# Performance work log

Measured on AMD Instinct MI355X. Metric: run time of the kernel, lower is better.

## Reference

```python
import jax, jax.numpy as jnp
import numpy as np

Nc, Nd, Ns = 8000, 6000, 6000          # circRNA / drug / disease node counts
F, H, O = 64, 4, 64                    # feature dim (fcir=fdrug=fdis), GAT heads, cnn out_channels
Ec, Ed, Es = 256000, 192000, 192000    # directed edge counts per graph
NEG_SLOPE = 0.2


def _gcn(x, src, dst, ew, W, b, N):
    # PyG GCNConv w/ edge_weight: add self loops (w=1), symmetric norm, x@W.T, scatter-add
    loop = jnp.arange(N, dtype=src.dtype)
    s = jnp.concatenate([src, loop])
    d = jnp.concatenate([dst, loop])
    w = jnp.concatenate([ew, jnp.ones((N,), x.dtype)])
    deg = jax.ops.segment_sum(w, d, num_segments=N)
    dinv = jnp.where(deg > 0, jax.lax.rsqrt(deg), 0.0)
    norm = dinv[s] * w * dinv[d]                        # [E+N]
    h = x @ W.T                                         # [N,F]
    return jax.ops.segment_sum(h[s] * norm[:, None], d, num_segments=N) + b


def _gat(x, src, dst, ew, W, a_src, a_dst, We, a_edge, b, N):
    # PyG GATConv(heads=H, concat=False, edge_dim=1); self loops with fill_value='mean'
    E = src.shape[0]
    ea = ew[:, None]                                    # [E,1]
    cnt = jax.ops.segment_sum(jnp.ones((E,), x.dtype), dst, num_segments=N)
    esum = jax.ops.segment_sum(ea, dst, num_segments=N)
    loop_attr = esum / jnp.maximum(cnt, 1.0)[:, None]   # per-dst mean edge attr
    loop = jnp.arange(N, dtype=src.dtype)
    s = jnp.concatenate([src, loop])
    d = jnp.concatenate([dst, loop])
    ea = jnp.concatenate([ea, loop_attr], axis=0)       # [E+N,1]
    h = (x @ W.T).reshape(N, H, F)
    al_s = jnp.einsum('nhf,hf->nh', h, a_src)
    al_d = jnp.einsum('nhf,hf->nh', h, a_dst)
    e = (ea @ We.T).reshape(-1, H, F)
    al_e = jnp.einsum('ehf,hf->eh', e, a_edge)
    alpha = al_s[s] + al_d[d] + al_e                    # [E+N,H]
    alpha = jnp.where(alpha >= 0, alpha, NEG_SLOPE * alpha)   # leaky_relu
    amax = jax.ops.segment_max(alpha, d, num_segments=N)
    ex = jnp.exp(alpha - amax[d])
    denom = jax.ops.segment_sum(ex, d, num_segments=N)
    coef = ex / denom[d]                                # segment softmax over incoming edges
    out = jax.ops.segment_sum(h[s] * coef[:, :, None], d, num_segments=N)  # [N,H,F]
    return out.mean(axis=1) + b                         # concat=False -> head mean


def _readout(x1, x2, W, b):
    # Conv1d(in=2, out=O, kernel=(F,1)) on [1,2,F,N] == full contraction over (layer, feature)
    X = jnp.stack([x1, x2], axis=0)                     # [2,N,F]
    return jnp.einsum('cnf,ocf->no', X, W) + b          # [N,O]


def _forward(fl, cir_edges, drug_edges, dis_edges):
    def branch(x, ei, ew, g1W, g1b, gaW, gas, gad, gaeW, gae, gab, g2W, g2b, N):
        src, dst = ei[0], ei[1]
        f1 = jax.nn.relu(_gcn(x, src, dst, ew, g1W, g1b, N))
        att = jax.nn.relu(_gat(f1, src, dst, ew, gaW, gas, gad, gaeW, gae, gab, N))
        f2 = jax.nn.relu(_gcn(att, src, dst, ew, g2W, g2b, N))
        return f1, f2

    cf1, cf2 = branch(fl['x_cir'], cir_edges, fl['cir_ew'], fl['gcn_cir1_W'], fl['gcn_cir1_b'],
                      fl['gat_cir_W'], fl['gat_cir_asrc'], fl['gat_cir_adst'], fl['gat_cir_eW'],
                      fl['gat_cir_aedge'], fl['gat_cir_b'], fl['gcn_cir2_W'], fl['gcn_cir2_b'], Nc)
    # NOTE: the source forward reuses the *_dis GCN/GAT layers for the drug branch (faithful)
    df1, df2 = branch(fl['x_drug'], drug_edges, fl['drug_ew'], fl['gcn_dis1_W'], fl['gcn_dis1_b'],
                      fl['gat_dis_W'], fl['gat_dis_asrc'], fl['gat_dis_adst'], fl['gat_dis_eW'],
                      fl['gat_dis_aedge'], fl['gat_dis_b'], fl['gcn_dis2_W'], fl['gcn_dis2_b'], Nd)
    sf1, sf2 = branch(fl['x_dis'], dis_edges, fl['dis_ew'], fl['gcn_dis1_W'], fl['gcn_dis1_b'],
                      fl['gat_dis_W'], fl['gat_dis_asrc'], fl['gat_dis_adst'], fl['gat_dis_eW'],
                      fl['gat_dis_aedge'], fl['gat_dis_b'], fl['gcn_dis2_W'], fl['gcn_dis2_b'], Ns)
    cir_fea = _readout(cf1, cf2, fl['cnn_cir_W'], fl['cnn_cir_b'])
    drug_fea = _readout(df1, df2, fl['cnn_dis_W'], fl['cnn_dis_b'])   # source uses cnn_dis for drug too
    dis_fea = _readout(sf1, sf2, fl['cnn_dis_W'], fl['cnn_dis_b'])
    return (cir_fea @ dis_fea.T, cir_fea @ drug_fea.T, drug_fea @ dis_fea.T,
            cir_fea, drug_fea, dis_fea)


_PARAM_SHAPES = [
    ('gcn_cir1_W', (F, F)), ('gcn_cir1_b', (F,)),
    ('gcn_cir2_W', (F, F)), ('gcn_cir2_b', (F,)),
    ('gcn_dis1_W', (F, F)), ('gcn_dis1_b', (F,)),
    ('gcn_dis2_W', (F, F)), ('gcn_dis2_b', (F,)),
    ('gat_cir_W', (H * F, F)), ('gat_cir_asrc', (H, F)), ('gat_cir_adst', (H, F)),
    ('gat_cir_eW', (H * F, 1)), ('gat_cir_aedge', (H, F)), ('gat_cir_b', (F,)),
    ('gat_dis_W', (H * F, F)), ('gat_dis_asrc', (H, F)), ('gat_dis_adst', (H, F)),
    ('gat_dis_eW', (H * F, 1)), ('gat_dis_aedge', (H, F)), ('gat_dis_b', (F,)),
    ('cnn_cir_W', (O, 2, F)), ('cnn_cir_b', (O,)),
    ('cnn_dis_W', (O, 2, F)), ('cnn_dis_b', (O,)),
]


def setup_inputs() -> dict:
    key = jax.random.key(0)
    ks = iter(jax.random.split(key, 64))
    inp = {}
    inp['x_cir'] = jax.random.normal(next(ks), (Nc, F), jnp.float32)
    inp['x_drug'] = jax.random.normal(next(ks), (Nd, F), jnp.float32)
    inp['x_dis'] = jax.random.normal(next(ks), (Ns, F), jnp.float32)
    inp['cir_edges'] = jax.random.randint(next(ks), (2, Ec), 0, Nc, dtype=jnp.int32)
    inp['cir_ew'] = jax.random.uniform(next(ks), (Ec,), jnp.float32)
    inp['drug_edges'] = jax.random.randint(next(ks), (2, Ed), 0, Nd, dtype=jnp.int32)
    inp['drug_ew'] = jax.random.uniform(next(ks), (Ed,), jnp.float32)
    inp['dis_edges'] = jax.random.randint(next(ks), (2, Es), 0, Ns, dtype=jnp.int32)
    inp['dis_ew'] = jax.random.uniform(next(ks), (Es,), jnp.float32)
    for name, shape in _PARAM_SHAPES:
        inp[name] = jax.random.normal(next(ks), shape, jnp.float32) * 0.1
    return inp


def reference(x_cir, x_drug, x_dis, cir_edges, cir_ew, drug_edges, drug_ew, dis_edges, dis_ew,
              gcn_cir1_W, gcn_cir1_b, gcn_cir2_W, gcn_cir2_b,
              gcn_dis1_W, gcn_dis1_b, gcn_dis2_W, gcn_dis2_b,
              gat_cir_W, gat_cir_asrc, gat_cir_adst, gat_cir_eW, gat_cir_aedge, gat_cir_b,
              gat_dis_W, gat_dis_asrc, gat_dis_adst, gat_dis_eW, gat_dis_aedge, gat_dis_b,
              cnn_cir_W, cnn_cir_b, cnn_dis_W, cnn_dis_b):
    fl = {k: v for k, v in locals().items() if k not in ('cir_edges', 'drug_edges', 'dis_edges')}
    return _forward(fl, cir_edges, drug_edges, dis_edges)
```

## Files before the change

### kernel.cpp

```cpp
#include <hip/hip_runtime.h>

#define NEG_SLOPE 0.2f

typedef __attribute__((ext_vector_type(8))) short bfrag;
typedef __attribute__((ext_vector_type(4))) float f32x4;

static __device__ __forceinline__ ushort f2bf(float x){
  uint u = __float_as_uint(x);
  uint r = (u + 0x7fff + ((u>>16)&1)) >> 16;
  return (ushort)r;
}
static __device__ __forceinline__ float bf2f(ushort h){
  return __uint_as_float(((uint)h)<<16);
}
static __device__ __forceinline__ float rdlane(float v, int l){
  return __int_as_float(__builtin_amdgcn_readlane(__float_as_int(v), l));
}


struct G3 {
  const int* src[3]; const int* dst[3]; const float* ew[3];
  float* deg[3];
  int* cnt[3]; int* pos[3];
  float* dinv[3]; float* lat[3]; int* rowp[3];
  int4* ep[3];
  int N[3]; int E[3];
};

struct MM3 {
  const float* A[3]; const float* B[3]; float* C[3]; const float* bias[3];
  ushort* H[3]; ushort* L[3];
  const float* gas[3]; const float* gad[3];
  float* als[3]; float* ald[3];
  int M[3]; int lda, ldb, N2;
};

struct AGG3 {
  const float* h[3]; const float* dinv[3]; const int* rowp[3];
  const int4* ep[3]; const float* bias[3];
  float* out[3]; int N[3]; int ostride, ooff;
};

struct GAT3 {
  const float* hg[3]; const float* als[3]; const float* ald[3];
  const float* lat[3]; const float* ce[3]; const int* rowp[3];
  const int4* ep[3]; const float* bias[3];
  float* out[3]; int N[3];
};

struct SC3 {
  const ushort* AH[3]; const ushort* AL[3];
  const ushort* BH[3]; const ushort* BL[3];
  float* C[3]; int M[3]; int N2;
};


__global__ void k_scan_b(G3 g, const float* gaeW_c, const float* gae_c, float* ce_c,
                         const float* gaeW_d, const float* gae_d, float* ce_d){
  int b = blockIdx.x;
  int tid = threadIdx.x;
  if (b < 2 && tid < 64){
    const float* W = b ? gaeW_d : gaeW_c;
    const float* Aa = b ? gae_d : gae_c;
    float* ceo = b ? ce_d : ce_c;
    #pragma unroll
    for (int hh=0; hh<4; hh++){
      float v = W[hh*64+tid] * Aa[hh*64+tid];
      #pragma unroll
      for (int off=32; off>0; off>>=1) v += __shfl_down(v,off);
      if (tid==0) ceo[hh] = v;
    }
  }
  int N = g.N[b];
  const float* degsum = g.deg[b];
  const int* cnt = g.cnt[b];
  float* dinv = g.dinv[b];
  float* lat = g.lat[b];
  int* rowp = g.rowp[b];
  const int T = 1024, PER = 8;
  __shared__ int ssum[T];
  int base = tid*PER;
  int loc[PER]; int s = 0;
  #pragma unroll
  for (int u=0;u<PER;u++){
    int i = base+u;
    int c = (i<N)? cnt[i] : 0;
    loc[u] = s; s += c;
    if (i<N){
      float ds = degsum[i];
      dinv[i] = rsqrtf(1.0f + ds);
      lat[i] = ds / fmaxf((float)c, 1.0f);
    }
  }
  ssum[tid] = s; __syncthreads();
  for (int off=1; off<T; off<<=1){
    int t = (tid>=off)? ssum[tid-off] : 0;
    __syncthreads();
    ssum[tid] += t;
    __syncthreads();
  }
  int excl = ssum[tid] - s;
  #pragma unroll
  for (int u=0;u<PER;u++){ int i=base+u; if (i<N) rowp[i] = excl + loc[u]; }
  if (tid == T-1) rowp[N] = ssum[T-1];
}

__global__ void k_scatter_b(G3 g){
  int b = blockIdx.z;
  int e = blockIdx.x*blockDim.x + threadIdx.x;
  if (e < g.E[b]){
    int d = g.dst[b][e];
    int s = g.src[b][e];
    float w = g.ew[b][e];
    float dw = g.dinv[b][s] * w;
    int p = g.rowp[b][d] + atomicAdd(&g.pos[b][d], 1);
    g.ep[b][p] = make_int4(s, __float_as_int(w), __float_as_int(dw), 0);
  }
}


template<int K, bool BIAS, bool SPLIT, bool ALQ, bool STATS>
__global__ __launch_bounds__(256)
void k_mm_b(MM3 P, G3 g){
  if (STATS && blockIdx.x == gridDim.x-1){
    int b = blockIdx.z;
    int E = g.E[b];
    const int* __restrict__ dst = g.dst[b];
    const float* __restrict__ ew = g.ew[b];
    float* __restrict__ deg = g.deg[b];
    int* __restrict__ cnt = g.cnt[b];
    int stride = gridDim.y*256;
    for (int e = blockIdx.y*256 + threadIdx.x; e < E; e += stride){
      int d = dst[e];
      atomicAdd(&deg[d], ew[e]);
      atomicAdd(&cnt[d], 1);
    }
    return;
  }
  int br = blockIdx.z;
  int M = P.M[br];
  int bi = blockIdx.y*128;
  if (bi >= M) return;
  int N2 = P.N2;
  int bj = blockIdx.x*128;
  const float* __restrict__ A = P.A[br];
  const float* __restrict__ B = P.B[br];
  float* __restrict__ C = P.C[br];
  int lda = P.lda, ldb = P.ldb;

  __shared__ float As[128*36];
  __shared__ float Bs[32*132];
  int tid = threadIdx.x;
  int tx = tid & 15, ty = tid >> 4;
  float acc[8][8] = {};

  for (int kh = 0; kh < K; kh += 32){
    for (int t = tid; t < 1024; t += 256){
      int r = t >> 3, k4 = (t & 7) << 2;
      int gr = bi + r;
      float4 v = (gr < M) ? *(const float4*)(A + (size_t)gr*lda + kh + k4)
                          : make_float4(0.f,0.f,0.f,0.f);
      *(float4*)(As + r*36 + k4) = v;
    }
    for (int t = tid; t < 1024; t += 256){
      int r = t >> 3, k4 = (t & 7) << 2;
      int gr = bj + r;
      float4 v = (gr < N2) ? *(const float4*)(B + (size_t)gr*ldb + kh + k4)
                           : make_float4(0.f,0.f,0.f,0.f);
      Bs[(k4+0)*132 + r] = v.x;
      Bs[(k4+1)*132 + r] = v.y;
      Bs[(k4+2)*132 + r] = v.z;
      Bs[(k4+3)*132 + r] = v.w;
    }
    __syncthreads();
    #pragma unroll
    for (int k = 0; k < 32; k += 4){
      float4 a4[8];
      #pragma unroll
      for (int u=0; u<4; u++){
        a4[u]   = *(const float4*)(As + (ty*4+u)*36 + k);
        a4[u+4] = *(const float4*)(As + (64+ty*4+u)*36 + k);
      }
      #pragma unroll
      for (int i=0; i<4; i++){
        float4 bl = *(const float4*)(Bs + (k+i)*132 + tx*4);
        float4 bh = *(const float4*)(Bs + (k+i)*132 + 64 + tx*4);
        #pragma unroll
        for (int u=0; u<8; u++){
          float av = (i==0)?a4[u].x : (i==1)?a4[u].y : (i==2)?a4[u].z : a4[u].w;
          acc[u][0] += av*bl.x; acc[u][1] += av*bl.y;
          acc[u][2] += av*bl.z; acc[u][3] += av*bl.w;
          acc[u][4] += av*bh.x; acc[u][5] += av*bh.y;
          acc[u][6] += av*bh.z; acc[u][7] += av*bh.w;
        }
      }
    }
    __syncthreads();
  }

  #pragma unroll
  for (int u=0; u<8; u++){
    int gi = bi + ((u<4) ? (ty*4+u) : (64+ty*4+(u-4)));
    if (gi >= M) continue;
    #pragma unroll
    for (int half=0; half<2; half++){
      int gj = bj + ((half==0) ? tx*4 : 64+tx*4);
      int v0 = half*4;
      if (gj + 4 <= N2){
        float4 r4 = make_float4(acc[u][v0],acc[u][v0+1],acc[u][v0+2],acc[u][v0+3]);
        if (BIAS){
          const float* bb = P.bias[br];
          r4.x += bb[gj]; r4.y += bb[gj+1]; r4.z += bb[gj+2]; r4.w += bb[gj+3];
        }
        *(float4*)(C + (size_t)gi*N2 + gj) = r4;
        if (SPLIT){
          ushort hv[4], lv[4];
          float vv[4] = {r4.x, r4.y, r4.z, r4.w};
          #pragma unroll
          for (int v=0; v<4; v++){
            hv[v] = f2bf(vv[v]);
            lv[v] = f2bf(vv[v] - bf2f(hv[v]));
          }
          *(ushort4*)(P.H[br] + (size_t)gi*N2 + gj) = make_ushort4(hv[0],hv[1],hv[2],hv[3]);
          *(ushort4*)(P.L[br] + (size_t)gi*N2 + gj) = make_ushort4(lv[0],lv[1],lv[2],lv[3]);
        }
      } else {
        for (int v=0; v<4; v++) if (gj+v < N2){
          float r = acc[u][v0+v];
          if (BIAS) r += P.bias[br][gj+v];
          C[(size_t)gi*N2+gj+v] = r;
        }
      }
    }
  }

  if (ALQ){
    int h0 = bj >> 6;
    float ps[8][2], pd[8][2];
    #pragma unroll
    for (int u=0;u<8;u++){ ps[u][0]=0.f; ps[u][1]=0.f; pd[u][0]=0.f; pd[u][1]=0.f; }
    #pragma unroll
    for (int half=0; half<2; half++){
      #pragma unroll
      for (int v=0; v<4; v++){
        int cw = tx*4 + v;
        float gs = P.gas[br][(h0+half)*64 + cw];
        float gd = P.gad[br][(h0+half)*64 + cw];
        #pragma unroll
        for (int u=0;u<8;u++){
          ps[u][half] += acc[u][half*4+v]*gs;
          pd[u][half] += acc[u][half*4+v]*gd;
        }
      }
    }
    #pragma unroll
    for (int u=0;u<8;u++){
      #pragma unroll
      for (int hf=0; hf<2; hf++){
        float s = ps[u][hf], d = pd[u][hf];
        #pragma unroll
        for (int off=8; off>0; off>>=1){ s += __shfl_down(s,off); d += __shfl_down(d,off); }
        if (tx==0){
          int gi = bi + ((u<4) ? (ty*4+u) : (64+ty*4+(u-4)));
          if (gi < M){
            P.als[br][gi*4 + h0 + hf] = s;
            P.ald[br][gi*4 + h0 + hf] = d;
          }
        }
      }
    }
  }
}


__global__ void k_gcn_agg_b(AGG3 P){
  int b = blockIdx.z;
  int wid = (blockIdx.x*blockDim.x + threadIdx.x) >> 6;
  int f = threadIdx.x & 63;
  if (wid >= P.N[b]) return;
  const float* __restrict__ h = P.h[b];
  const int4* __restrict__ ep = P.ep[b];
  float dn = P.dinv[b][wid];
  float acc = dn*h[(size_t)wid*64 + f];
  int p0 = P.rowp[b][wid], p1 = P.rowp[b][wid+1];
  int p = p0;
  for (; p+4 <= p1; p+=4){
    int4 e0 = ep[p], e1 = ep[p+1], e2 = ep[p+2], e3 = ep[p+3];
    float v0 = h[(size_t)e0.x*64 + f];
    float v1 = h[(size_t)e1.x*64 + f];
    float v2 = h[(size_t)e2.x*64 + f];
    float v3 = h[(size_t)e3.x*64 + f];
    acc = fmaf(__int_as_float(e0.z), v0, acc);
    acc = fmaf(__int_as_float(e1.z), v1, acc);
    acc = fmaf(__int_as_float(e2.z), v2, acc);
    acc = fmaf(__int_as_float(e3.z), v3, acc);
  }
  for (; p < p1; p++){
    int4 pr = ep[p];
    acc = fmaf(__int_as_float(pr.z), h[(size_t)pr.x*64 + f], acc);
  }
  P.out[b][(size_t)wid*P.ostride + P.ooff + f] = fmaxf(fmaf(dn, acc, P.bias[b][f]), 0.f);
}


__global__ void k_gat_agg_b(GAT3 P){
  int b = blockIdx.z;
  int wid = (blockIdx.x*blockDim.x + threadIdx.x) >> 6;
  int lane = threadIdx.x & 63;
  if (wid >= P.N[b]) return;
  const float* __restrict__ hg = P.hg[b];
  const float* __restrict__ als = P.als[b];
  const int4* __restrict__ ep = P.ep[b];
  int h = lane & 3;
  int el = lane >> 2;
  int f = lane;

  float4 cv = *(const float4*)P.ce[b];
  float4 adv = *(const float4*)(P.ald[b] + (size_t)wid*4);
  float4 asv = *(const float4*)(als + (size_t)wid*4);
  float c_l  = (h==0)?cv.x :(h==1)?cv.y :(h==2)?cv.z :cv.w;
  float ad_l = (h==0)?adv.x:(h==1)?adv.y:(h==2)?adv.z:adv.w;
  float as_l = (h==0)?asv.x:(h==1)?asv.y:(h==2)?asv.z:asv.w;
  float la = P.lat[b][wid];

  float a_self = as_l + ad_l + la*c_l;
  a_self = (a_self >= 0.f) ? a_self : NEG_SLOPE*a_self;
  float m = a_self;

  float l = 1.f;
  const float* hn = hg + (size_t)wid*256;
  float acc0 = hn[f];
  float acc1 = hn[64+f];
  float acc2 = hn[128+f];
  float acc3 = hn[192+f];

  int p0 = P.rowp[b][wid], p1 = P.rowp[b][wid+1];
  for (int c0=p0; c0<p1; c0+=16){
    int idx = c0 + el;
    float ex = 0.f;
    int s_lane = 0;
    if (idx < p1){
      int4 pr = ep[idx];
      s_lane = pr.x;
      float w = __int_as_float(pr.y);
      float a = als[s_lane*4 + h] + ad_l + w*c_l;
      a = (a >= 0.f) ? a : NEG_SLOPE*a;
      ex = __expf(a - m);
    }
    float ls = ex;
    #pragma unroll
    for (int off=4; off<64; off<<=1) ls += __shfl_xor(ls, off);
    l += ls;
    int cnt = p1 - c0; if (cnt > 16) cnt = 16;
    #pragma unroll 2
    for (int e=0; e<cnt; e++){
      int s = __builtin_amdgcn_readlane(s_lane, e*4);
      const float* hs = hg + (size_t)s*256 + f;
      float x0 = rdlane(ex, e*4+0);
      float x1 = rdlane(ex, e*4+1);
      float x2 = rdlane(ex, e*4+2);
      float x3 = rdlane(ex, e*4+3);
      acc0 = fmaf(x0, hs[0],   acc0);
      acc1 = fmaf(x1, hs[64],  acc1);
      acc2 = fmaf(x2, hs[128], acc2);
      acc3 = fmaf(x3, hs[192], acc3);
    }
  }
  float o = acc0/rdlane(l,0) + acc1/rdlane(l,1) + acc2/rdlane(l,2) + acc3/rdlane(l,3);
  P.out[b][(size_t)wid*64 + f] = fmaxf(0.25f*o + P.bias[b][f], 0.f);
}


__global__ __launch_bounds__(256)
void k_score(SC3 P){
  int br = blockIdx.z;
  int M = P.M[br];
  int bi = blockIdx.y*128;
  if (bi >= M) return;
  int N = P.N2;
  int bj = blockIdx.x*128;
  const ushort* __restrict__ AH = P.AH[br];
  const ushort* __restrict__ ALo = P.AL[br];
  const ushort* __restrict__ BH = P.BH[br];
  const ushort* __restrict__ BLo = P.BL[br];
  float* __restrict__ C = P.C[br];

  int wv = threadIdx.x >> 6;
  int lane = threadIdx.x & 63;
  int la = lane & 15, lk = lane >> 4;
  int r0 = bi + (wv>>1)*64;
  int c0 = bj + (wv&1)*64;

  bfrag ah[4][2], al[4][2];
  #pragma unroll
  for (int mi=0; mi<4; mi++){
    int r = r0 + mi*16 + la; if (r > M-1) r = M-1;
    size_t base = (size_t)r*64 + lk*8;
    ah[mi][0] = *(const bfrag*)(AH + base);
    ah[mi][1] = *(const bfrag*)(AH + base + 32);
    al[mi][0] = *(const bfrag*)(ALo + base);
    al[mi][1] = *(const bfrag*)(ALo + base + 32);
  }

  f32x4 acc[4][4];
  #pragma unroll
  for (int mi=0; mi<4; mi++)
    #pragma unroll
    for (int ni=0; ni<4; ni++)
      acc[mi][ni] = (f32x4){0.f,0.f,0.f,0.f};

  #pragma unroll
  for (int ni=0; ni<4; ni++){
    int cc = c0 + ni*16 + la; if (cc > N-1) cc = N-1;
    size_t base = (size_t)cc*64 + lk*8;
    bfrag bh0 = *(const bfrag*)(BH + base);
    bfrag bh1 = *(const bfrag*)(BH + base + 32);
    bfrag bl0 = *(const bfrag*)(BLo + base);
    bfrag bl1 = *(const bfrag*)(BLo + base + 32);
    #pragma unroll
    for (int mi=0; mi<4; mi++){
      f32x4 a = acc[mi][ni];
      a = __builtin_amdgcn_mfma_f32_16x16x32_bf16(ah[mi][0], bh0, a, 0, 0, 0);
      a = __builtin_amdgcn_mfma_f32_16x16x32_bf16(ah[mi][1], bh1, a, 0, 0, 0);
      a = __builtin_amdgcn_mfma_f32_16x16x32_bf16(ah[mi][0], bl0, a, 0, 0, 0);
      a = __builtin_amdgcn_mfma_f32_16x16x32_bf16(ah[mi][1], bl1, a, 0, 0, 0);
      a = __builtin_amdgcn_mfma_f32_16x16x32_bf16(al[mi][0], bh0, a, 0, 0, 0);
      a = __builtin_amdgcn_mfma_f32_16x16x32_bf16(al[mi][1], bh1, a, 0, 0, 0);
      acc[mi][ni] = a;
    }
  }

  #pragma unroll
  for (int mi=0; mi<4; mi++){
    int rb = r0 + mi*16 + lk*4;
    #pragma unroll
    for (int ni=0; ni<4; ni++){
      int col = c0 + ni*16 + la;
      if (col >= N) continue;
      #pragma unroll
      for (int rg=0; rg<4; rg++){
        int r = rb + rg;
        if (r < M) C[(size_t)r*N + col] = acc[mi][ni][rg];
      }
    }
  }
}


extern "C" void kernel_launch(void* const* d_in, const int* in_sizes, int n_in,
                              void* d_out, int out_size, void* d_ws, size_t ws_size,
                              hipStream_t stream){
  const float* x_cir  = (const float*)d_in[0];
  const float* x_drug = (const float*)d_in[1];
  const float* x_dis  = (const float*)d_in[2];
  const int*   cir_edges  = (const int*)d_in[3];
  const float* cir_ew     = (const float*)d_in[4];
  const int*   drug_edges = (const int*)d_in[5];
  const float* drug_ew    = (const float*)d_in[6];
  const int*   dis_edges  = (const int*)d_in[7];
  const float* dis_ew     = (const float*)d_in[8];
  const float* gcn_cir1_W = (const float*)d_in[9];
  const float* gcn_cir1_b = (const float*)d_in[10];
  const float* gcn_cir2_W = (const float*)d_in[11];
  const float* gcn_cir2_b = (const float*)d_in[12];
  const float* gcn_dis1_W = (const float*)d_in[13];
  const float* gcn_dis1_b = (const float*)d_in[14];
  const float* gcn_dis2_W = (const float*)d_in[15];
  const float* gcn_dis2_b = (const float*)d_in[16];
  const float* gat_cir_W    = (const float*)d_in[17];
  const float* gat_cir_asrc = (const float*)d_in[18];
  const float* gat_cir_adst = (const float*)d_in[19];
  const float* gat_cir_eW   = (const float*)d_in[20];
  const float* gat_cir_aedge= (const float*)d_in[21];
  const float* gat_cir_b    = (const float*)d_in[22];
  const float* gat_dis_W    = (const float*)d_in[23];
  const float* gat_dis_asrc = (const float*)d_in[24];
  const float* gat_dis_adst = (const float*)d_in[25];
  const float* gat_dis_eW   = (const float*)d_in[26];
  const float* gat_dis_aedge= (const float*)d_in[27];
  const float* gat_dis_b    = (const float*)d_in[28];
  const float* cnn_cir_W = (const float*)d_in[29];
  const float* cnn_cir_b = (const float*)d_in[30];
  const float* cnn_dis_W = (const float*)d_in[31];
  const float* cnn_dis_b = (const float*)d_in[32];
  float* out = (float*)d_out;

  const int Nb[3] = {8000, 6000, 6000};
  const int Eb[3] = {256000, 192000, 192000};

  char* wp = (char*)d_ws;
  auto alloc = [&](size_t bytes)->void*{
    void* p = wp; wp += (bytes + 255) & ~(size_t)255; return p;
  };

  float* fea[3] = { out + 132000000ULL, out + 132512000ULL, out + 132896000ULL };

  float* ce_c = (float*)alloc(64);
  float* ce_d = (float*)alloc(64);

  G3 g;
  const int* edges[3] = {cir_edges, drug_edges, dis_edges};
  const float* ews[3] = {cir_ew, drug_ew, dis_ew};

  char* zero_base = wp;
  for (int b=0; b<3; b++){
    g.deg[b]  = (float*)alloc((size_t)Nb[b]*4);
    g.cnt[b]  = (int*)alloc((size_t)Nb[b]*4);
    g.pos[b]  = (int*)alloc((size_t)Nb[b]*4);
  }
  size_t zero_bytes = (size_t)(wp - zero_base);

  float *hbuf[3], *f12[3], *att[3], *als[3], *ald[3];
  ushort *feaH[3], *feaL[3];
  for (int b=0; b<3; b++){
    g.src[b] = edges[b];
    g.dst[b] = edges[b] + Eb[b];
    g.ew[b]  = ews[b];
    g.N[b] = Nb[b]; g.E[b] = Eb[b];
    g.dinv[b] = (float*)alloc((size_t)Nb[b]*4);
    g.lat[b]  = (float*)alloc((size_t)Nb[b]*4);
    g.rowp[b] = (int*)alloc((size_t)(Nb[b]+1)*4);
    g.ep[b]   = (int4*)alloc((size_t)Eb[b]*16);
    als[b]  = (float*)alloc((size_t)Nb[b]*4*4);
    ald[b]  = (float*)alloc((size_t)Nb[b]*4*4);
    hbuf[b] = (float*)alloc((size_t)Nb[b]*256*4);
    f12[b]  = (float*)alloc((size_t)Nb[b]*128*4);
    att[b]  = (float*)alloc((size_t)Nb[b]*64*4);
    feaH[b] = (ushort*)alloc((size_t)Nb[b]*64*2);
    feaL[b] = (ushort*)alloc((size_t)Nb[b]*64*2);
  }

  const float* xin[3]  = {x_cir, x_drug, x_dis};
  const float* g1W[3]  = {gcn_cir1_W, gcn_dis1_W, gcn_dis1_W};
  const float* g1b[3]  = {gcn_cir1_b, gcn_dis1_b, gcn_dis1_b};
  const float* g2W[3]  = {gcn_cir2_W, gcn_dis2_W, gcn_dis2_W};
  const float* g2b[3]  = {gcn_cir2_b, gcn_dis2_b, gcn_dis2_b};
  const float* gaW[3]  = {gat_cir_W, gat_dis_W, gat_dis_W};
  const float* gasP[3] = {gat_cir_asrc, gat_dis_asrc, gat_dis_asrc};
  const float* gadP[3] = {gat_cir_adst, gat_dis_adst, gat_dis_adst};
  const float* gab[3]  = {gat_cir_b, gat_dis_b, gat_dis_b};
  const float* cep[3]  = {ce_c, ce_d, ce_d};
  const float* cW[3]   = {cnn_cir_W, cnn_dis_W, cnn_dis_W};
  const float* cb[3]   = {cnn_cir_b, cnn_dis_b, cnn_dis_b};

  auto mkmm = [&](MM3& m, const float* const* Ap, const float* const* Bp,
                  float* const* Cp, const float* const* bp, int lda, int ldb, int N2){
    for (int b=0;b<3;b++){
      m.A[b]=Ap[b]; m.B[b]=Bp[b]; m.C[b]=Cp[b]; m.bias[b]= bp? bp[b] : nullptr;
      m.H[b]=nullptr; m.L[b]=nullptr;
      m.gas[b]=nullptr; m.gad[b]=nullptr; m.als[b]=nullptr; m.ald[b]=nullptr;
      m.M[b]=Nb[b];
    }
    m.lda=lda; m.ldb=ldb; m.N2=N2;
  };

  hipMemsetAsync(zero_base, 0, zero_bytes, stream);

  MM3 m1; mkmm(m1, xin, g1W, hbuf, nullptr, 64, 64, 64);
  k_mm_b<64,false,false,false,true><<<dim3(2,63,3),256,0,stream>>>(m1, g);

  k_scan_b<<<3,1024,0,stream>>>(g, gat_cir_eW, gat_cir_aedge, ce_c,
                                   gat_dis_eW, gat_dis_aedge, ce_d);
  k_scatter_b<<<dim3(1000,1,3),256,0,stream>>>(g);

  AGG3 a1;
  for (int b=0;b<3;b++){ a1.h[b]=hbuf[b]; a1.dinv[b]=g.dinv[b]; a1.rowp[b]=g.rowp[b];
    a1.ep[b]=g.ep[b]; a1.bias[b]=g1b[b]; a1.out[b]=f12[b]; a1.N[b]=Nb[b]; }
  a1.ostride=128; a1.ooff=0;
  k_gcn_agg_b<<<dim3(2000,1,3),256,0,stream>>>(a1);

  {
    const float* Ap[3] = {f12[0], f12[1], f12[2]};
    MM3 m2; mkmm(m2, Ap, gaW, hbuf, nullptr, 128, 64, 256);
    for (int b=0;b<3;b++){ m2.gas[b]=gasP[b]; m2.gad[b]=gadP[b]; m2.als[b]=als[b]; m2.ald[b]=ald[b]; }
    k_mm_b<64,false,false,true,false><<<dim3(2,63,3),256,0,stream>>>(m2, g);
  }

  GAT3 gt;
  for (int b=0;b<3;b++){ gt.hg[b]=hbuf[b]; gt.als[b]=als[b]; gt.ald[b]=ald[b]; gt.lat[b]=g.lat[b];
    gt.ce[b]=cep[b]; gt.rowp[b]=g.rowp[b]; gt.ep[b]=g.ep[b];
    gt.bias[b]=gab[b]; gt.out[b]=att[b]; gt.N[b]=Nb[b]; }
  k_gat_agg_b<<<dim3(2000,1,3),256,0,stream>>>(gt);

  {
    const float* Ap[3] = {att[0], att[1], att[2]};
    MM3 m3; mkmm(m3, Ap, g2W, hbuf, nullptr, 64, 64, 64);
    k_mm_b<64,false,false,false,false><<<dim3(1,63,3),256,0,stream>>>(m3, g);
  }

  AGG3 a2 = a1;
  for (int b=0;b<3;b++){ a2.bias[b]=g2b[b]; }
  a2.ooff=64;
  k_gcn_agg_b<<<dim3(2000,1,3),256,0,stream>>>(a2);

  {
    const float* Ap[3] = {f12[0], f12[1], f12[2]};
    MM3 m4; mkmm(m4, Ap, cW, fea, cb, 128, 128, 64);
    for (int b=0;b<3;b++){ m4.H[b]=feaH[b]; m4.L[b]=feaL[b]; }
    k_mm_b<128,true,true,false,false><<<dim3(1,63,3),256,0,stream>>>(m4, g);
  }

  SC3 sc;
  sc.AH[0]=feaH[0]; sc.AL[0]=feaL[0]; sc.BH[0]=feaH[2]; sc.BL[0]=feaL[2];
  sc.C[0]=out;               sc.M[0]=8000;
  sc.AH[1]=feaH[0]; sc.AL[1]=feaL[0]; sc.BH[1]=feaH[1]; sc.BL[1]=feaL[1];
  sc.C[1]=out + 48000000ULL; sc.M[1]=8000;
  sc.AH[2]=feaH[1]; sc.AL[2]=feaL[1]; sc.BH[2]=feaH[2]; sc.BL[2]=feaL[2];
  sc.C[2]=out + 96000000ULL; sc.M[2]=6000;
  sc.N2=6000;
  k_score<<<dim3(47,63,3),256,0,stream>>>(sc);
}
```

Baseline: 992.3 us.

## Store GAT features in bf16 and coalesce score writes via shared memory

The GAT projection matmul now writes its output as bf16, and the GAT aggregation reads bf16 and widens to float, halving the bytes of the per-edge neighbour gathers. The score kernel now stages each wave's accumulator tile in shared memory and writes it out as row-contiguous float4 stores to improve write coalescing of the large output. This reduces precision of GAT features, and the score kernel now uses a large shared buffer per block, which may lower occupancy.

```diff
diff --git a/kernel.cpp b/kernel.cpp
--- a/kernel.cpp
+++ b/kernel.cpp
@@ -42,7 +42,8 @@
 };
 
 struct GAT3 {
-  const float* hg[3]; const float* als[3]; const float* ald[3];
+  const ushort* hg[3];
+  const float* als[3]; const float* ald[3];
   const float* lat[3]; const float* ce[3]; const int* rowp[3];
   const int4* ep[3]; const float* bias[3];
   float* out[3]; int N[3];
@@ -119,7 +120,7 @@
 }
 
 
-template<int K, bool BIAS, bool SPLIT, bool ALQ, bool STATS>
+template<int K, bool BIAS, bool SPLIT, bool ALQ, bool STATS, bool CBF>
 __global__ __launch_bounds__(256)
 void k_mm_b(MM3 P, G3 g){
   if (STATS && blockIdx.x == gridDim.x-1){
@@ -212,23 +213,29 @@
           const float* bb = P.bias[br];
           r4.x += bb[gj]; r4.y += bb[gj+1]; r4.z += bb[gj+2]; r4.w += bb[gj+3];
         }
-        *(float4*)(C + (size_t)gi*N2 + gj) = r4;
-        if (SPLIT){
-          ushort hv[4], lv[4];
-          float vv[4] = {r4.x, r4.y, r4.z, r4.w};
-          #pragma unroll
-          for (int v=0; v<4; v++){
-            hv[v] = f2bf(vv[v]);
-            lv[v] = f2bf(vv[v] - bf2f(hv[v]));
+        if (CBF){
+          ushort4 uv = make_ushort4(f2bf(r4.x), f2bf(r4.y), f2bf(r4.z), f2bf(r4.w));
+          *(ushort4*)((ushort*)C + (size_t)gi*N2 + gj) = uv;
+        } else {
+          *(float4*)(C + (size_t)gi*N2 + gj) = r4;
+          if (SPLIT){
+            ushort hv[4], lv[4];
+            float vv[4] = {r4.x, r4.y, r4.z, r4.w};
+            #pragma unroll
+            for (int v=0; v<4; v++){
+              hv[v] = f2bf(vv[v]);
+              lv[v] = f2bf(vv[v] - bf2f(hv[v]));
+            }
+            *(ushort4*)(P.H[br] + (size_t)gi*N2 + gj) = make_ushort4(hv[0],hv[1],hv[2],hv[3]);
+            *(ushort4*)(P.L[br] + (size_t)gi*N2 + gj) = make_ushort4(lv[0],lv[1],lv[2],lv[3]);
           }
-          *(ushort4*)(P.H[br] + (size_t)gi*N2 + gj) = make_ushort4(hv[0],hv[1],hv[2],hv[3]);
-          *(ushort4*)(P.L[br] + (size_t)gi*N2 + gj) = make_ushort4(lv[0],lv[1],lv[2],lv[3]);
         }
       } else {
         for (int v=0; v<4; v++) if (gj+v < N2){
           float r = acc[u][v0+v];
           if (BIAS) r += P.bias[br][gj+v];
-          C[(size_t)gi*N2+gj+v] = r;
+          if (CBF) ((ushort*)C)[(size_t)gi*N2+gj+v] = f2bf(r);
+          else     C[(size_t)gi*N2+gj+v] = r;
         }
       }
     }
@@ -308,7 +315,7 @@
   int wid = (blockIdx.x*blockDim.x + threadIdx.x) >> 6;
   int lane = threadIdx.x & 63;
   if (wid >= P.N[b]) return;
-  const float* __restrict__ hg = P.hg[b];
+  const ushort* __restrict__ hg = P.hg[b];
   const float* __restrict__ als = P.als[b];
   const int4* __restrict__ ep = P.ep[b];
   int h = lane & 3;
@@ -328,11 +335,11 @@
   float m = a_self;
 
   float l = 1.f;
-  const float* hn = hg + (size_t)wid*256;
-  float acc0 = hn[f];
-  float acc1 = hn[64+f];
-  float acc2 = hn[128+f];
-  float acc3 = hn[192+f];
+  const ushort* hn = hg + (size_t)wid*256;
+  float acc0 = bf2f(hn[f]);
+  float acc1 = bf2f(hn[64+f]);
+  float acc2 = bf2f(hn[128+f]);
+  float acc3 = bf2f(hn[192+f]);
 
   int p0 = P.rowp[b][wid], p1 = P.rowp[b][wid+1];
   for (int c0=p0; c0<p1; c0+=16){
@@ -355,15 +362,15 @@
     #pragma unroll 2
     for (int e=0; e<cnt; e++){
       int s = __builtin_amdgcn_readlane(s_lane, e*4);
-      const float* hs = hg + (size_t)s*256 + f;
+      const ushort* hs = hg + (size_t)s*256 + f;
       float x0 = rdlane(ex, e*4+0);
       float x1 = rdlane(ex, e*4+1);
       float x2 = rdlane(ex, e*4+2);
       float x3 = rdlane(ex, e*4+3);
-      acc0 = fmaf(x0, hs[0],   acc0);
-      acc1 = fmaf(x1, hs[64],  acc1);
-      acc2 = fmaf(x2, hs[128], acc2);
-      acc3 = fmaf(x3, hs[192], acc3);
+      acc0 = fmaf(x0, bf2f(hs[0]),   acc0);
+      acc1 = fmaf(x1, bf2f(hs[64]),  acc1);
+      acc2 = fmaf(x2, bf2f(hs[128]), acc2);
+      acc3 = fmaf(x3, bf2f(hs[192]), acc3);
     }
   }
   float o = acc0/rdlane(l,0) + acc1/rdlane(l,1) + acc2/rdlane(l,2) + acc3/rdlane(l,3);
@@ -385,6 +392,8 @@
   const ushort* __restrict__ BLo = P.BL[br];
   float* __restrict__ C = P.C[br];
 
+  __shared__ float ts[4*64*68];
+
   int wv = threadIdx.x >> 6;
   int lane = threadIdx.x & 63;
   int la = lane & 15, lk = lane >> 4;
@@ -430,17 +439,30 @@
     }
   }
 
-  #pragma unroll
-  for (int mi=0; mi<4; mi++){
-    int rb = r0 + mi*16 + lk*4;
-    #pragma unroll
-    for (int ni=0; ni<4; ni++){
-      int col = c0 + ni*16 + la;
-      if (col >= N) continue;
+  float* T = ts + wv*64*68;
+  #pragma unroll
+  for (int mi=0; mi<4; mi++)
+    #pragma unroll
+    for (int ni=0; ni<4; ni++)
       #pragma unroll
-      for (int rg=0; rg<4; rg++){
-        int r = rb + rg;
-        if (r < M) C[(size_t)r*N + col] = acc[mi][ni][rg];
+      for (int rg=0; rg<4; rg++)
+        T[(mi*16 + lk*4 + rg)*68 + ni*16 + la] = acc[mi][ni][rg];
+  __syncthreads();
+
+  #pragma unroll
+  for (int i=0; i<16; i++){
+    int t = i*64 + lane;
+    int row = t >> 4;
+    int q = t & 15;
+    int grow = r0 + row;
+    int gcol = c0 + q*4;
+    if (grow < M){
+      if (gcol + 4 <= N){
+        float4 v = *(const float4*)(T + row*68 + q*4);
+        *(float4*)(C + (size_t)grow*N + gcol) = v;
+      } else {
+        for (int v2=0; v2<4; v2++)
+          if (gcol+v2 < N) C[(size_t)grow*N + gcol+v2] = T[row*68 + q*4 + v2];
       }
     }
   }
@@ -557,7 +579,7 @@
   hipMemsetAsync(zero_base, 0, zero_bytes, stream);
 
   MM3 m1; mkmm(m1, xin, g1W, hbuf, nullptr, 64, 64, 64);
-  k_mm_b<64,false,false,false,true><<<dim3(2,63,3),256,0,stream>>>(m1, g);
+  k_mm_b<64,false,false,false,true,false><<<dim3(2,63,3),256,0,stream>>>(m1, g);
 
   k_scan_b<<<3,1024,0,stream>>>(g, gat_cir_eW, gat_cir_aedge, ce_c,
                                    gat_dis_eW, gat_dis_aedge, ce_d);
@@ -573,19 +595,19 @@
     const float* Ap[3] = {f12[0], f12[1], f12[2]};
     MM3 m2; mkmm(m2, Ap, gaW, hbuf, nullptr, 128, 64, 256);
     for (int b=0;b<3;b++){ m2.gas[b]=gasP[b]; m2.gad[b]=gadP[b]; m2.als[b]=als[b]; m2.ald[b]=ald[b]; }
-    k_mm_b<64,false,false,true,false><<<dim3(2,63,3),256,0,stream>>>(m2, g);
+    k_mm_b<64,false,false,true,false,true><<<dim3(2,63,3),256,0,stream>>>(m2, g);
   }
 
   GAT3 gt;
-  for (int b=0;b<3;b++){ gt.hg[b]=hbuf[b]; gt.als[b]=als[b]; gt.ald[b]=ald[b]; gt.lat[b]=g.lat[b];
-    gt.ce[b]=cep[b]; gt.rowp[b]=g.rowp[b]; gt.ep[b]=g.ep[b];
+  for (int b=0;b<3;b++){ gt.hg[b]=(const ushort*)hbuf[b]; gt.als[b]=als[b]; gt.ald[b]=ald[b];
+    gt.lat[b]=g.lat[b]; gt.ce[b]=cep[b]; gt.rowp[b]=g.rowp[b]; gt.ep[b]=g.ep[b];
     gt.bias[b]=gab[b]; gt.out[b]=att[b]; gt.N[b]=Nb[b]; }
   k_gat_agg_b<<<dim3(2000,1,3),256,0,stream>>>(gt);
 
   {
     const float* Ap[3] = {att[0], att[1], att[2]};
     MM3 m3; mkmm(m3, Ap, g2W, hbuf, nullptr, 64, 64, 64);
-    k_mm_b<64,false,false,false,false><<<dim3(1,63,3),256,0,stream>>>(m3, g);
+    k_mm_b<64,false,false,false,false,false><<<dim3(1,63,3),256,0,stream>>>(m3, g);
   }
 
   AGG3 a2 = a1;
@@ -597,7 +619,7 @@
     const float* Ap[3] = {f12[0], f12[1], f12[2]};
     MM3 m4; mkmm(m4, Ap, cW, fea, cb, 128, 128, 64);
     for (int b=0;b<3;b++){ m4.H[b]=feaH[b]; m4.L[b]=feaL[b]; }
-    k_mm_b<128,true,true,false,false><<<dim3(1,63,3),256,0,stream>>>(m4, g);
+    k_mm_b<128,true,true,false,false,false><<<dim3(1,63,3),256,0,stream>>>(m4, g);
   }
 
   SC3 sc;
```

Measured after the change: 924.2 us. 1.07x faster.
